# Kernel tuning notes

Hardware: AMD Instinct MI355X
Metric: run time of the kernel (lower is better)

The kernel has to match this reference:

```python
import jax, jax.numpy as jnp
import numpy as np

N_NODES = 50000
N_EDGES = 800000
D = 128
H = 8
HD = D // H
N_NTYPES = 3
N_ETYPES = 5
LN_EPS = 1e-5


def setup_inputs() -> dict:
    key = jax.random.key(0)
    ks = jax.random.split(key, 16)
    inp = {
        "x": jax.random.normal(ks[0], (N_NODES, D), dtype=jnp.float32),
        "edge_index": jax.random.randint(ks[1], (2, N_EDGES), 0, N_NODES),
        "edge_type": jax.random.randint(ks[2], (N_EDGES,), 0, N_ETYPES),
        "node_type": jax.random.randint(ks[3], (N_NODES,), 0, N_NTYPES),
        # per-(node_type, head) QKV projections, per-(edge_type, head) K transform
        "W_Q": jax.random.normal(ks[4], (N_NTYPES, H, HD, HD), dtype=jnp.float32) * 0.02,
        "W_K": jax.random.normal(ks[5], (N_NTYPES, H, HD, HD), dtype=jnp.float32) * 0.02,
        "W_V": jax.random.normal(ks[6], (N_NTYPES, H, HD, HD), dtype=jnp.float32) * 0.02,
        "W_edge": jax.random.normal(ks[7], (N_ETYPES, H, HD, HD), dtype=jnp.float32) * 0.02,
        "mu": jnp.ones((H, N_ETYPES), dtype=jnp.float32),
        "W_out": jax.random.normal(ks[8], (D, D), dtype=jnp.float32) * 0.02,
        "b_out": jnp.zeros((D,), dtype=jnp.float32),
        "ln1_g": jnp.ones((D,), dtype=jnp.float32),
        "ln1_b": jnp.zeros((D,), dtype=jnp.float32),
        "W1": jax.random.normal(ks[9], (D, 4 * D), dtype=jnp.float32) * 0.02,
        "b1": jnp.zeros((4 * D,), dtype=jnp.float32),
        "W2": jax.random.normal(ks[10], (4 * D, D), dtype=jnp.float32) * 0.02,
        "b2": jnp.zeros((D,), dtype=jnp.float32),
        "ln2_g": jnp.ones((D,), dtype=jnp.float32),
        "ln2_b": jnp.zeros((D,), dtype=jnp.float32),
    }
    return inp


def _layer_norm(y, g, b):
    m = y.mean(-1, keepdims=True)
    v = ((y - m) ** 2).mean(-1, keepdims=True)
    return (y - m) * jax.lax.rsqrt(v + LN_EPS) * g + b


def reference(x, edge_index, edge_type, node_type,
              W_Q, W_K, W_V, W_edge, mu,
              W_out, b_out, ln1_g, ln1_b, W1, b1, W2, b2, ln2_g, ln2_b):
    N = x.shape[0]
    xh = x.reshape(N, H, HD)  # heads vectorized (concat of per-head slices)

    # type-specific QKV: small fixed loop over node types, masked select
    Q = jnp.zeros_like(xh)
    K = jnp.zeros_like(xh)
    V = jnp.zeros_like(xh)
    for t in range(N_NTYPES):
        m = (node_type == t)[:, None, None]
        Q = jnp.where(m, jnp.einsum('nhd,hdf->nhf', xh, W_Q[t]), Q)
        K = jnp.where(m, jnp.einsum('nhd,hdf->nhf', xh, W_K[t]), K)
        V = jnp.where(m, jnp.einsum('nhd,hdf->nhf', xh, W_V[t]), V)

    src, dst = edge_index[0], edge_index[1]
    q_dst = Q[dst]   # [E,H,HD]
    k_src = K[src]   # [E,H,HD]

    # edge-type-specific K transform
    kt = jnp.zeros_like(k_src)
    for et in range(N_ETYPES):
        m = (edge_type == et)[:, None, None]
        kt = jnp.where(m, jnp.einsum('ehd,hdf->ehf', k_src, W_edge[et]), kt)

    scores = (q_dst * kt).sum(-1) / jnp.sqrt(jnp.float32(HD))  # [E,H]
    scores = scores * mu[:, edge_type].T                       # mu per edge type, per head

    # sparse softmax over incoming edges of each dst node, per head
    smax = jax.ops.segment_max(scores, dst, num_segments=N)
    ex = jnp.exp(scores - smax[dst])
    den = jax.ops.segment_sum(ex, dst, num_segments=N)
    w = ex / (den[dst] + 1e-10)                                 # [E,H]

    agg = jax.ops.segment_sum(V[src] * w[..., None], dst, num_segments=N)  # [N,H,HD]
    mh = agg.reshape(N, D) @ W_out + b_out  # dropout is identity in eval

    h = _layer_norm(x + mh, ln1_g, ln1_b)
    ffn = jax.nn.gelu(h @ W1 + b1, approximate=False) @ W2 + b2
    return _layer_norm(h + ffn, ln2_g, ln2_b)
```

## Files before the change

### kernel.cpp

```cpp
#include <hip/hip_runtime.h>
#include <hip/hip_bf16.h>

#define N_NODESC 50000
#define N_EDGESC 800000
#define DD 128
#define HH 8
#define HDIM 16
#define N_NT 3
#define N_ET 5
#define NPB 196
#define NEB 400
#define NFB 512

#define KV8_OFF    ((size_t)0)
#define QT8_OFF    ((size_t)12800000)
#define XP_OFF     ((size_t)44800000)
#define AGG_OFF    ((size_t)57600000)
#define WOUTT_OFF  ((size_t)83200000)
#define W1T_OFF    ((size_t)83232768)
#define W2T_OFF    ((size_t)83363840)
#define WALL_OFF   ((size_t)83494912)
#define EDATA_OFF  ((size_t)84183040)
#define ROWS_OFF   ((size_t)87383040)
#define ORIG_OFF   ((size_t)87583104)
#define DEG_OFF    ((size_t)87783104)
#define TOFS_OFF   ((size_t)87983104)
#define BH_OFF     ((size_t)87983168)
#define BB_OFF     ((size_t)87985536)
#define TMP_OFF    ((size_t)87988928)
#define RLOC_OFF   ((size_t)91188928)
#define CSUM_OFF   ((size_t)91389056)

using short8 = __attribute__((ext_vector_type(8))) short;
using f32x4  = __attribute__((ext_vector_type(4))) float;
using f32x2  = __attribute__((ext_vector_type(2))) float;

__device__ __forceinline__ ushort f2b(float f) {
    __hip_bfloat16 h = __float2bfloat16(f);
    return *(ushort*)&h;
}
__device__ __forceinline__ float b2f(ushort u) {
    __hip_bfloat16 h = *(__hip_bfloat16*)&u;
    return __bfloat162float(h);
}
__device__ __forceinline__ f32x2 pk0(unsigned int w) {
    return __builtin_amdgcn_cvt_pk_f32_fp8((int)w, false);
}
__device__ __forceinline__ f32x2 pk1(unsigned int w) {
    return __builtin_amdgcn_cvt_pk_f32_fp8((int)w, true);
}
__device__ __forceinline__ float gelu_f(float v) {
    return 0.5f * v * (1.f + erff(v * 0.70710678118654752f));
}

__global__ __launch_bounds__(256) void prep_a(
    const float* __restrict__ Wout, const float* __restrict__ W1, const float* __restrict__ W2,
    const float* __restrict__ WQ, const float* __restrict__ Wk, const float* __restrict__ Wv,
    const float* __restrict__ We, const float* __restrict__ mu,
    ushort* __restrict__ Woutt, ushort* __restrict__ W1t, ushort* __restrict__ W2t,
    ushort* __restrict__ Wall,
    const int* __restrict__ ntype, int* __restrict__ bh,
    const int* __restrict__ dst, int* __restrict__ deg, unsigned int* __restrict__ tmp)
{
    const int b = blockIdx.x, tid = threadIdx.x;
    if (b < 1920) {
        const int gid = b * 256 + tid;
        if (gid < 16384) {
            const int nn = gid >> 7, k = gid & 127;
            Woutt[gid] = f2b(Wout[k * 128 + nn]);
        } else if (gid < 81920) {
            const int i = gid - 16384;
            const int nn = i >> 7, k = i & 127;
            W1t[i] = f2b(W1[k * 512 + nn]);
        } else if (gid < 147456) {
            const int i = gid - 81920;
            const int nn = i >> 9, k = i & 511;
            W2t[i] = f2b(W2[k * 128 + nn]);
        } else {
            const int idx = gid - 147456;
            const int t = idx / (896 * 128);
            const int rem = idx % (896 * 128);
            const int c = rem / 128, k = rem % 128;
            const int hk = k >> 4, ck = k & 15;
            float v = 0.f;
            if (c < 128) {
                const int hc = c >> 4, j = c & 15;
                if (hk == hc) v = 4.f * Wk[((t * HH + hc) * HDIM + ck) * HDIM + j];
            } else if (c < 256) {
                const int c2 = c - 128, hc = c2 >> 4, j = c2 & 15;
                if (hk == hc) v = 4.f * Wv[((t * HH + hc) * HDIM + ck) * HDIM + j];
            } else {
                const int cq = c - 256, et = cq >> 7, dd = cq & 127;
                const int hq = dd >> 4, j = dd & 15;
                if (hk == hq) {
                    const float* wq = WQ + ((t * HH + hq) * HDIM + ck) * HDIM;
                    const float* we = We + ((et * HH + hq) * HDIM + j) * HDIM;
                    float s = 0.f;
#pragma unroll
                    for (int f = 0; f < 16; f++) s = fmaf(wq[f], we[f], s);
                    v = 64.f * mu[hq * N_ET + et] * s;
                }
            }
            Wall[idx] = f2b(v);
        }
    } else if (b < 1920 + NPB) {
        const int bc = b - 1920;
        const int wave = tid >> 6, lane = tid & 63;
        const int n = bc * 256 + tid;
        const int t = (n < N_NODESC) ? ntype[n] : -1;
        const unsigned long long m0 = __ballot(t == 0);
        const unsigned long long m1 = __ballot(t == 1);
        const unsigned long long m2 = __ballot(t == 2);
        __shared__ int wcnt[4][3];
        if (lane == 0) {
            wcnt[wave][0] = (int)__popcll(m0);
            wcnt[wave][1] = (int)__popcll(m1);
            wcnt[wave][2] = (int)__popcll(m2);
        }
        __syncthreads();
        if (tid < 3)
            bh[tid * NPB + bc] = wcnt[0][tid] + wcnt[1][tid] + wcnt[2][tid] + wcnt[3][tid];
    } else {
        for (int e = (b - 1920 - NPB) * 256 + tid; e < N_EDGESC; e += NEB * 256) {
            const int nd = dst[e];
            const unsigned int p = (unsigned int)atomicAdd(&deg[nd], 1);
            tmp[e] = (p << 16) | (unsigned int)nd;
        }
    }
}

__global__ __launch_bounds__(256) void prep_b(
    const int* __restrict__ bh, const int* __restrict__ deg,
    int* __restrict__ bb, int* __restrict__ tofs,
    int* __restrict__ rloc, int* __restrict__ csum)
{
    __shared__ int part[256];
    const int tid = threadIdx.x;
    if (blockIdx.x == 0) {
        const int base3 = tid * 3;
        int e0 = (base3 + 0 < 588) ? bh[base3 + 0] : 0;
        int e1 = (base3 + 1 < 588) ? bh[base3 + 1] : 0;
        int e2 = (base3 + 2 < 588) ? bh[base3 + 2] : 0;
        const int l0 = e0, l1 = e0 + e1, l2 = l1 + e2;
        part[tid] = l2;
        __syncthreads();
        for (int off = 1; off < 256; off <<= 1) {
            const int u = (tid >= off) ? part[tid - off] : 0;
            __syncthreads();
            part[tid] += u;
            __syncthreads();
        }
        const int tb = part[tid] - l2;
        if (base3 + 0 < 588) bb[base3 + 0] = tb;
        if (base3 + 1 < 588) bb[base3 + 1] = tb + l0;
        if (base3 + 2 < 588) bb[base3 + 2] = tb + l1;
        __syncthreads();
        if (tid == 0) {
            tofs[0] = 0;
            tofs[1] = bb[NPB];
            tofs[2] = bb[2 * NPB];
            tofs[3] = N_NODESC;
        }
    } else {
        const int c = blockIdx.x - 1;
        const int n = c * 256 + tid;
        const int vdeg = (n < N_NODESC) ? deg[n] : 0;
        part[tid] = vdeg;
        __syncthreads();
        for (int off = 1; off < 256; off <<= 1) {
            const int u = (tid >= off) ? part[tid - off] : 0;
            __syncthreads();
            part[tid] += u;
            __syncthreads();
        }
        if (n <= N_NODESC) rloc[n] = part[tid] - vdeg;
        if (tid == 255) csum[c] = part[255];
    }
}

__global__ __launch_bounds__(256) void prep_c(
    const int* __restrict__ ntype, const float* __restrict__ x,
    const int* __restrict__ src, const int* __restrict__ etype,
    const int* __restrict__ bb, const int* __restrict__ rloc, const int* __restrict__ csum,
    const unsigned int* __restrict__ tmp,
    int* __restrict__ origof, ushort* __restrict__ Xp, int* __restrict__ rows,
    int* __restrict__ edata)
{
    const int b = blockIdx.x, tid = threadIdx.x;
    __shared__ int cb[256];
    {
        const int v = (tid < NPB) ? csum[tid] : 0;
        cb[tid] = v;
        __syncthreads();
        for (int off = 1; off < 256; off <<= 1) {
            const int u = (tid >= off) ? cb[tid - off] : 0;
            __syncthreads();
            cb[tid] += u;
            __syncthreads();
        }
        const int incl = cb[tid];
        __syncthreads();
        cb[tid] = incl - v;
        __syncthreads();
    }

    if (b < NPB) {
        const int wave = tid >> 6, lane = tid & 63;
        const int n = b * 256 + tid;
        const int t = (n < N_NODESC) ? ntype[n] : -1;
        const unsigned long long m0 = __ballot(t == 0);
        const unsigned long long m1 = __ballot(t == 1);
        const unsigned long long m2 = __ballot(t == 2);
        __shared__ int wcnt[4][3];
        __shared__ int sp[256];
        if (lane == 0) {
            wcnt[wave][0] = (int)__popcll(m0);
            wcnt[wave][1] = (int)__popcll(m1);
            wcnt[wave][2] = (int)__popcll(m2);
        }
        __syncthreads();
        int p = -1;
        if (n < N_NODESC) {
            int basew = 0;
#pragma unroll
            for (int w = 0; w < 4; w++) if (w < wave) basew += wcnt[w][t];
            const unsigned long long mt = (t == 0) ? m0 : (t == 1) ? m1 : m2;
            const unsigned long long mlt = ((unsigned long long)1 << lane) - 1;
            p = bb[t * NPB + b] + basew + (int)__popcll(mt & mlt);
            origof[p] = n;
        }
        if (n <= N_NODESC) rows[n] = cb[b] + rloc[n];
        sp[tid] = p;
        __syncthreads();
        for (int i = tid; i < 256 * 16; i += 256) {
            const int nn = i >> 4, c = (i & 15) << 3;
            const int pp = sp[nn];
            if (pp < 0) continue;
            const int n2 = b * 256 + nn;
            const float4 v0 = *(const float4*)(x + (size_t)n2 * DD + c);
            const float4 v1 = *(const float4*)(x + (size_t)n2 * DD + c + 4);
            ushort o[8] = {f2b(v0.x), f2b(v0.y), f2b(v0.z), f2b(v0.w),
                           f2b(v1.x), f2b(v1.y), f2b(v1.z), f2b(v1.w)};
            *(uint4*)(Xp + (size_t)pp * DD + c) = *(uint4*)o;
        }
    } else {
        for (int e = (b - NPB) * 256 + tid; e < N_EDGESC; e += NFB * 256) {
            const unsigned int v = tmp[e];
            const int nd = (int)(v & 0xffffu);
            const int p = (int)(v >> 16);
            edata[cb[nd >> 8] + rloc[nd] + p] = src[e] | (etype[e] << 16);
        }
    }
}

#define LDP 36

__global__ __launch_bounds__(256) void proj_gemm(
    const ushort* __restrict__ Xp, const ushort* __restrict__ Wall,
    const int* __restrict__ tofs, const int* __restrict__ origof,
    ushort* __restrict__ KV8, unsigned char* __restrict__ Qt8)
{
    const int t = blockIdx.z;
    const int rs = tofs[t], re = tofs[t + 1];
    const int mBase = rs + blockIdx.x * 128;
    if (mBase >= re) return;
    const int nBase = blockIdx.y * 128;
    const ushort* Bt = Wall + (size_t)t * 896 * 128;

    __shared__ ushort As[128 * LDP];
    __shared__ ushort Bs[128 * LDP];
    const int tid = threadIdx.x;
    const int lane = tid & 63, wave = tid >> 6;
    const int mw = (wave >> 1) * 64, nw = (wave & 1) * 64;
    const int l15 = lane & 15, q8 = (lane >> 4) * 8;

    f32x4 acc[4][4];
#pragma unroll
    for (int i = 0; i < 4; i++)
#pragma unroll
        for (int j = 0; j < 4; j++) acc[i][j] = (f32x4){0.f, 0.f, 0.f, 0.f};

    const int r0 = tid >> 2, c0 = (tid & 3) * 8;
    int rA0 = mBase + r0;      if (rA0 >= N_NODESC) rA0 = N_NODESC - 1;
    int rA1 = mBase + r0 + 64; if (rA1 >= N_NODESC) rA1 = N_NODESC - 1;

    for (int kk = 0; kk < 128; kk += 32) {
        short8 a0 = *(const short8*)(Xp + (size_t)rA0 * DD + kk + c0);
        short8 a1 = *(const short8*)(Xp + (size_t)rA1 * DD + kk + c0);
        short8 b0 = *(const short8*)(Bt + (size_t)(nBase + r0) * 128 + kk + c0);
        short8 b1 = *(const short8*)(Bt + (size_t)(nBase + r0 + 64) * 128 + kk + c0);
        *(short8*)&As[r0 * LDP + c0] = a0;
        *(short8*)&As[(r0 + 64) * LDP + c0] = a1;
        *(short8*)&Bs[r0 * LDP + c0] = b0;
        *(short8*)&Bs[(r0 + 64) * LDP + c0] = b1;
        __syncthreads();
        short8 af[4], bf[4];
#pragma unroll
        for (int i = 0; i < 4; i++)
            af[i] = *(const short8*)&As[(mw + i * 16 + l15) * LDP + q8];
#pragma unroll
        for (int j = 0; j < 4; j++)
            bf[j] = *(const short8*)&Bs[(nw + j * 16 + l15) * LDP + q8];
#pragma unroll
        for (int i = 0; i < 4; i++)
#pragma unroll
            for (int j = 0; j < 4; j++)
                acc[i][j] = __builtin_amdgcn_mfma_f32_16x16x32_bf16(af[i], bf[j], acc[i][j], 0, 0, 0);
        __syncthreads();
    }

    unsigned char* kvb = (unsigned char*)KV8;
    const int rq = (lane >> 4) * 4;
#pragma unroll
    for (int i = 0; i < 4; i++) {
#pragma unroll
        for (int r = 0; r < 4; r++) {
            const int gm = mBase + mw + i * 16 + rq + r;
            if (gm >= re) continue;
            const int og = origof[gm];
#pragma unroll
            for (int j = 0; j < 4; j++) {
                const int gn = nBase + nw + j * 16 + l15;
                const float v = acc[i][j][r];
                const unsigned char b8 =
                    (unsigned char)(__builtin_amdgcn_cvt_pk_fp8_f32(v, v, 0, false) & 0xff);
                if (gn < 256) kvb[(size_t)og * 256 + gn] = b8;
                else          Qt8[(size_t)og * 640 + (gn - 256)] = b8;
            }
        }
    }
}

__global__ __launch_bounds__(128) void edgeagg_kernel(
    const int* __restrict__ rowstart, const int* __restrict__ edata,
    const unsigned char* __restrict__ Qt8, const unsigned char* __restrict__ KV8,
    ushort* __restrict__ agg)
{
    const int w = threadIdx.x >> 6;
    const int lane = threadIdx.x & 63;
    const int n = blockIdx.x * 2 + w;
    const int slot = lane >> 3;
    const int h = lane & 7;

    __shared__ uint4 qs8s[2][40];
    if (lane < 40)
        qs8s[w][lane] = ((const uint4*)(Qt8 + (size_t)n * 640))[lane];
    __syncthreads();
    const uint* qbase = (const uint*)&qs8s[w][0];

    const int s0 = rowstart[n], s1 = rowstart[n + 1];
    const float qsc = 1.44269504f / 1024.f;

    float acc[16];
#pragma unroll
    for (int j = 0; j < 16; j++) acc[j] = 0.f;
    float den = 0.f;

    for (int i = s0 + slot; i < s1; i += 8) {
        const int ed = edata[i];
        const int sn = ed & 0xffff;
        const int et = ed >> 16;
        const unsigned char* kvp = KV8 + ((size_t)sn << 8);
        const uint4 kw = *(const uint4*)(kvp + (h << 4));
        const uint4 vw = *(const uint4*)(kvp + 128 + (h << 4));
        const uint4 qw = *(const uint4*)(qbase + (et << 5) + (h << 2));

        const f32x2 q0 = pk0(qw.x), q1 = pk1(qw.x), q2 = pk0(qw.y), q3 = pk1(qw.y);
        const f32x2 q4 = pk0(qw.z), q5 = pk1(qw.z), q6 = pk0(qw.w), q7 = pk1(qw.w);
        const f32x2 k0 = pk0(kw.x), k1 = pk1(kw.x), k2 = pk0(kw.y), k3 = pk1(kw.y);
        const f32x2 k4 = pk0(kw.z), k5 = pk1(kw.z), k6 = pk0(kw.w), k7 = pk1(kw.w);

        float pa = q0.x * k0.x;
        float pb = q0.y * k0.y;
        float pc = q1.x * k1.x;
        float pd = q1.y * k1.y;
        pa = fmaf(q2.x, k2.x, pa); pb = fmaf(q2.y, k2.y, pb);
        pc = fmaf(q3.x, k3.x, pc); pd = fmaf(q3.y, k3.y, pd);
        pa = fmaf(q4.x, k4.x, pa); pb = fmaf(q4.y, k4.y, pb);
        pc = fmaf(q5.x, k5.x, pc); pd = fmaf(q5.y, k5.y, pd);
        pa = fmaf(q6.x, k6.x, pa); pb = fmaf(q6.y, k6.y, pb);
        pc = fmaf(q7.x, k7.x, pc); pd = fmaf(q7.y, k7.y, pd);

        const float ex = exp2f(((pa + pb) + (pc + pd)) * qsc);
        den += ex;

        const f32x2 v0 = pk0(vw.x), v1 = pk1(vw.x), v2 = pk0(vw.y), v3 = pk1(vw.y);
        const f32x2 v4 = pk0(vw.z), v5 = pk1(vw.z), v6 = pk0(vw.w), v7 = pk1(vw.w);
        acc[0]  = fmaf(ex, v0.x, acc[0]);  acc[1]  = fmaf(ex, v0.y, acc[1]);
        acc[2]  = fmaf(ex, v1.x, acc[2]);  acc[3]  = fmaf(ex, v1.y, acc[3]);
        acc[4]  = fmaf(ex, v2.x, acc[4]);  acc[5]  = fmaf(ex, v2.y, acc[5]);
        acc[6]  = fmaf(ex, v3.x, acc[6]);  acc[7]  = fmaf(ex, v3.y, acc[7]);
        acc[8]  = fmaf(ex, v4.x, acc[8]);  acc[9]  = fmaf(ex, v4.y, acc[9]);
        acc[10] = fmaf(ex, v5.x, acc[10]); acc[11] = fmaf(ex, v5.y, acc[11]);
        acc[12] = fmaf(ex, v6.x, acc[12]); acc[13] = fmaf(ex, v6.y, acc[13]);
        acc[14] = fmaf(ex, v7.x, acc[14]); acc[15] = fmaf(ex, v7.y, acc[15]);
    }

    {
        const int b0 = slot & 1, b1 = slot & 2, b2 = slot & 4;
#pragma unroll
        for (int j = 0; j < 8; j++) {
            const float v = b0 ? acc[j] : acc[j + 8];
            const float r = __shfl_xor(v, 8);
            acc[j] = (b0 ? acc[j + 8] : acc[j]) + r;
        }
#pragma unroll
        for (int j = 0; j < 4; j++) {
            const float v = b1 ? acc[j] : acc[j + 4];
            const float r = __shfl_xor(v, 16);
            acc[j] = (b1 ? acc[j + 4] : acc[j]) + r;
        }
#pragma unroll
        for (int j = 0; j < 2; j++) {
            const float v = b2 ? acc[j] : acc[j + 2];
            const float r = __shfl_xor(v, 32);
            acc[j] = (b2 ? acc[j + 2] : acc[j]) + r;
        }
        den += __shfl_xor(den, 8);
        den += __shfl_xor(den, 16);
        den += __shfl_xor(den, 32);
    }
    const float rr = 0.25f / (den + 1e-10f);
    const int fb = (h << 4) + ((slot & 1) << 3) + ((slot & 2) << 1) + ((slot & 4) >> 1);
    ushort o2[2] = { f2b(acc[0] * rr), f2b(acc[1] * rr) };
    *(uint*)&agg[((size_t)n << 7) + fb] = *(uint*)o2;
}

#define LDH 132

__global__ __launch_bounds__(256) void fused_tail(
    const ushort* __restrict__ agg, const ushort* __restrict__ Woutt,
    const ushort* __restrict__ W1t, const ushort* __restrict__ W2t,
    const float* __restrict__ x,
    const float* __restrict__ bout, const float* __restrict__ g1, const float* __restrict__ b1ln,
    const float* __restrict__ b1, const float* __restrict__ b2,
    const float* __restrict__ g2, const float* __restrict__ b2ln,
    float* __restrict__ out)
{
    __shared__ ushort Hs[64 * LDH];
    __shared__ ushort As[64 * LDP];
    __shared__ ushort Bs[128 * LDP];
    __shared__ float red[2][2][64];

    const int tid = threadIdx.x;
    const int lane = tid & 63, wave = tid >> 6;
    const int wm = wave >> 1, wn = wave & 1;
    const int l15 = lane & 15, q8 = (lane >> 4) * 8, rq = (lane >> 4) * 4;
    const int mBase = blockIdx.x * 64;

    const int rA = tid >> 2, c0 = (tid & 3) * 8;
    int rowA = mBase + rA; if (rowA >= N_NODESC) rowA = N_NODESC - 1;

    f32x4 acc1[2][4], acc2[2][4];
#pragma unroll
    for (int i = 0; i < 2; i++)
#pragma unroll
        for (int j = 0; j < 4; j++) {
            acc1[i][j] = (f32x4){0.f, 0.f, 0.f, 0.f};
            acc2[i][j] = (f32x4){0.f, 0.f, 0.f, 0.f};
        }

    for (int kk = 0; kk < 128; kk += 32) {
        short8 a0 = *(const short8*)(agg + (size_t)rowA * DD + kk + c0);
        short8 b0 = *(const short8*)(Woutt + (size_t)rA * 128 + kk + c0);
        short8 b1r = *(const short8*)(Woutt + (size_t)(rA + 64) * 128 + kk + c0);
        *(short8*)&As[rA * LDP + c0] = a0;
        *(short8*)&Bs[rA * LDP + c0] = b0;
        *(short8*)&Bs[(rA + 64) * LDP + c0] = b1r;
        __syncthreads();
        short8 af[2], bf[4];
#pragma unroll
        for (int i = 0; i < 2; i++)
            af[i] = *(const short8*)&As[(wm * 32 + i * 16 + l15) * LDP + q8];
#pragma unroll
        for (int j = 0; j < 4; j++)
            bf[j] = *(const short8*)&Bs[(wn * 64 + j * 16 + l15) * LDP + q8];
#pragma unroll
        for (int i = 0; i < 2; i++)
#pragma unroll
            for (int j = 0; j < 4; j++)
                acc1[i][j] = __builtin_amdgcn_mfma_f32_16x16x32_bf16(af[i], bf[j], acc1[i][j], 0, 0, 0);
        __syncthreads();
    }

    {
        float boutv[4], gv[4], bv[4];
#pragma unroll
        for (int j = 0; j < 4; j++) {
            const int gn = wn * 64 + j * 16 + l15;
            boutv[j] = bout[gn]; gv[j] = g1[gn]; bv[j] = b1ln[gn];
        }
#pragma unroll
        for (int i = 0; i < 2; i++) {
#pragma unroll
            for (int r = 0; r < 4; r++) {
                const int row = wm * 32 + i * 16 + rq + r;
                const int gm = mBase + row;
                float s = 0.f, ss = 0.f;
#pragma unroll
                for (int j = 0; j < 4; j++) {
                    const int gn = wn * 64 + j * 16 + l15;
                    float v = acc1[i][j][r] + boutv[j];
                    v += (gm < N_NODESC) ? x[(size_t)gm * DD + gn] : 0.f;
                    acc1[i][j][r] = v;
                    s += v; ss += v * v;
                }
                s  += __shfl_xor(s, 1);  s  += __shfl_xor(s, 2);  s  += __shfl_xor(s, 4);  s  += __shfl_xor(s, 8);
                ss += __shfl_xor(ss, 1); ss += __shfl_xor(ss, 2); ss += __shfl_xor(ss, 4); ss += __shfl_xor(ss, 8);
                if (l15 == 0) { red[0][wn][row] = s; red[1][wn][row] = ss; }
            }
        }
        __syncthreads();
#pragma unroll
        for (int i = 0; i < 2; i++) {
#pragma unroll
            for (int r = 0; r < 4; r++) {
                const int row = wm * 32 + i * 16 + rq + r;
                const float s  = red[0][0][row] + red[0][1][row];
                const float ss = red[1][0][row] + red[1][1][row];
                const float mean = s * (1.f / 128.f);
                const float var  = ss * (1.f / 128.f) - mean * mean;
                const float rstd = rsqrtf(var + 1e-5f);
#pragma unroll
                for (int j = 0; j < 4; j++) {
                    const int gn = wn * 64 + j * 16 + l15;
                    const float o = (acc1[i][j][r] - mean) * rstd * gv[j] + bv[j];
                    Hs[row * LDH + gn] = f2b(o);
                }
            }
        }
        __syncthreads();
    }

    for (int nb = 0; nb < 4; nb++) {
#pragma unroll
        for (int i = 0; i < 2; i++)
#pragma unroll
            for (int j = 0; j < 4; j++) acc1[i][j] = (f32x4){0.f, 0.f, 0.f, 0.f};

        for (int kk = 0; kk < 128; kk += 32) {
            short8 b0 = *(const short8*)(W1t + (size_t)(nb * 128 + rA) * 128 + kk + c0);
            short8 b1r = *(const short8*)(W1t + (size_t)(nb * 128 + rA + 64) * 128 + kk + c0);
            *(short8*)&Bs[rA * LDP + c0] = b0;
            *(short8*)&Bs[(rA + 64) * LDP + c0] = b1r;
            __syncthreads();
            short8 af[2], bf[4];
#pragma unroll
            for (int i = 0; i < 2; i++)
                af[i] = *(const short8*)&Hs[(wm * 32 + i * 16 + l15) * LDH + kk + q8];
#pragma unroll
            for (int j = 0; j < 4; j++)
                bf[j] = *(const short8*)&Bs[(wn * 64 + j * 16 + l15) * LDP + q8];
#pragma unroll
            for (int i = 0; i < 2; i++)
#pragma unroll
                for (int j = 0; j < 4; j++)
                    acc1[i][j] = __builtin_amdgcn_mfma_f32_16x16x32_bf16(af[i], bf[j], acc1[i][j], 0, 0, 0);
            __syncthreads();
        }

        float b1v[4];
#pragma unroll
        for (int j = 0; j < 4; j++)
            b1v[j] = b1[nb * 128 + wn * 64 + j * 16 + l15];

        for (int kk2 = 0; kk2 < 4; kk2++) {
            short8 b0 = *(const short8*)(W2t + (size_t)rA * 512 + nb * 128 + kk2 * 32 + c0);
            short8 b1r = *(const short8*)(W2t + (size_t)(rA + 64) * 512 + nb * 128 + kk2 * 32 + c0);
            *(short8*)&Bs[rA * LDP + c0] = b0;
            *(short8*)&Bs[(rA + 64) * LDP + c0] = b1r;
            if (wn == (kk2 >> 1)) {
                const int j0 = 2 * (kk2 & 1);
#pragma unroll
                for (int i = 0; i < 2; i++)
#pragma unroll
                    for (int jj = 0; jj < 2; jj++)
#pragma unroll
                        for (int r = 0; r < 4; r++) {
                            const int row = wm * 32 + i * 16 + rq + r;
                            const float v = gelu_f(acc1[i][j0 + jj][r] + b1v[j0 + jj]);
                            As[row * LDP + jj * 16 + l15] = f2b(v);
                        }
            }
            __syncthreads();
            short8 af[2], bf[4];
#pragma unroll
            for (int i = 0; i < 2; i++)
                af[i] = *(const short8*)&As[(wm * 32 + i * 16 + l15) * LDP + q8];
#pragma unroll
            for (int j = 0; j < 4; j++)
                bf[j] = *(const short8*)&Bs[(wn * 64 + j * 16 + l15) * LDP + q8];
#pragma unroll
            for (int i = 0; i < 2; i++)
#pragma unroll
                for (int j = 0; j < 4; j++)
                    acc2[i][j] = __builtin_amdgcn_mfma_f32_16x16x32_bf16(af[i], bf[j], acc2[i][j], 0, 0, 0);
            __syncthreads();
        }
    }

    {
        float b2v[4], gv[4], bv[4];
#pragma unroll
        for (int j = 0; j < 4; j++) {
            const int gn = wn * 64 + j * 16 + l15;
            b2v[j] = b2[gn]; gv[j] = g2[gn]; bv[j] = b2ln[gn];
        }
#pragma unroll
        for (int i = 0; i < 2; i++) {
#pragma unroll
            for (int r = 0; r < 4; r++) {
                const int row = wm * 32 + i * 16 + rq + r;
                float s = 0.f, ss = 0.f;
#pragma unroll
                for (int j = 0; j < 4; j++) {
                    const int gn = wn * 64 + j * 16 + l15;
                    float v = acc2[i][j][r] + b2v[j] + b2f(Hs[row * LDH + gn]);
                    acc2[i][j][r] = v;
                    s += v; ss += v * v;
                }
                s  += __shfl_xor(s, 1);  s  += __shfl_xor(s, 2);  s  += __shfl_xor(s, 4);  s  += __shfl_xor(s, 8);
                ss += __shfl_xor(ss, 1); ss += __shfl_xor(ss, 2); ss += __shfl_xor(ss, 4); ss += __shfl_xor(ss, 8);
                if (l15 == 0) { red[0][wn][row] = s; red[1][wn][row] = ss; }
            }
        }
        __syncthreads();
#pragma unroll
        for (int i = 0; i < 2; i++) {
#pragma unroll
            for (int r = 0; r < 4; r++) {
                const int row = wm * 32 + i * 16 + rq + r;
                const int gm = mBase + row;
                if (gm >= N_NODESC) continue;
                const float s  = red[0][0][row] + red[0][1][row];
                const float ss = red[1][0][row] + red[1][1][row];
                const float mean = s * (1.f / 128.f);
                const float var  = ss * (1.f / 128.f) - mean * mean;
                const float rstd = rsqrtf(var + 1e-5f);
#pragma unroll
                for (int j = 0; j < 4; j++) {
                    const int gn = wn * 64 + j * 16 + l15;
                    out[(size_t)gm * DD + gn] = (acc2[i][j][r] - mean) * rstd * gv[j] + bv[j];
                }
            }
        }
    }
}

extern "C" void kernel_launch(void* const* d_in, const int* in_sizes, int n_in,
                              void* d_out, int out_size, void* d_ws, size_t ws_size,
                              hipStream_t stream)
{
    const float* x     = (const float*)d_in[0];
    const int*   ei    = (const int*)d_in[1];
    const int*   etyp  = (const int*)d_in[2];
    const int*   ntype = (const int*)d_in[3];
    const float* Wq    = (const float*)d_in[4];
    const float* Wk    = (const float*)d_in[5];
    const float* Wv    = (const float*)d_in[6];
    const float* We    = (const float*)d_in[7];
    const float* mu    = (const float*)d_in[8];
    const float* Wout  = (const float*)d_in[9];
    const float* bout  = (const float*)d_in[10];
    const float* g1    = (const float*)d_in[11];
    const float* b1ln  = (const float*)d_in[12];
    const float* W1    = (const float*)d_in[13];
    const float* b1    = (const float*)d_in[14];
    const float* W2    = (const float*)d_in[15];
    const float* b2    = (const float*)d_in[16];
    const float* g2    = (const float*)d_in[17];
    const float* b2ln  = (const float*)d_in[18];
    float* out = (float*)d_out;

    char* ws = (char*)d_ws;
    ushort*        KV8   = (ushort*)(ws + KV8_OFF);
    unsigned char* Qt8   = (unsigned char*)(ws + QT8_OFF);
    ushort*        Xp    = (ushort*)(ws + XP_OFF);
    ushort*        agg   = (ushort*)(ws + AGG_OFF);
    ushort*        Woutt = (ushort*)(ws + WOUTT_OFF);
    ushort*        W1t   = (ushort*)(ws + W1T_OFF);
    ushort*        W2t   = (ushort*)(ws + W2T_OFF);
    ushort*        Wall  = (ushort*)(ws + WALL_OFF);
    int*           edata = (int*)(ws + EDATA_OFF);
    int*           rows  = (int*)(ws + ROWS_OFF);
    int*           origof= (int*)(ws + ORIG_OFF);
    int*           deg   = (int*)(ws + DEG_OFF);
    int*           tofs  = (int*)(ws + TOFS_OFF);
    int*           bh    = (int*)(ws + BH_OFF);
    int*           bb    = (int*)(ws + BB_OFF);
    unsigned int*  tmp   = (unsigned int*)(ws + TMP_OFF);
    int*           rloc  = (int*)(ws + RLOC_OFF);
    int*           csum  = (int*)(ws + CSUM_OFF);

    const int* srcA = ei;
    const int* dstA = ei + N_EDGESC;

    (void)hipMemsetAsync(ws + DEG_OFF, 0, 200000, stream);

    prep_a<<<1920 + NPB + NEB, 256, 0, stream>>>(
        Wout, W1, W2, Wq, Wk, Wv, We, mu, Woutt, W1t, W2t, Wall,
        ntype, bh, dstA, deg, tmp);
    prep_b<<<1 + NPB, 256, 0, stream>>>(bh, deg, bb, tofs, rloc, csum);
    prep_c<<<NPB + NFB, 256, 0, stream>>>(ntype, x, srcA, etyp, bb, rloc, csum, tmp,
                                          origof, Xp, rows, edata);

    proj_gemm<<<dim3(394, 7, 3), 256, 0, stream>>>(Xp, Wall, tofs, origof, KV8, Qt8);
    edgeagg_kernel<<<N_NODESC / 2, 128, 0, stream>>>(rows, edata, Qt8,
                                                     (const unsigned char*)KV8, agg);

    fused_tail<<<782, 256, 0, stream>>>(agg, Woutt, W1t, W2t, x,
                                        bout, g1, b1ln, b1, b2, g2, b2ln, out);
}
```

Baseline: 342.4 us.

## Prefetch next weight tiles into registers and stage full GELU tile in LDS

Restructures the fused tail kernel so each k-step issues the global loads for the next weight/agg tile into registers before computing on the current LDS tile. The loads chain across the Wout, W1 and W2 phases. Barriers become a custom ebar that waits only on LDS counters, leaving global loads in flight across it. The GELU output of each W1 block is written to a new full 64x128 Ts buffer in one pass instead of half-tile slices per W2 step. This costs more LDS and can lower occupancy.

```diff
diff --git a/kernel.cpp b/kernel.cpp
--- a/kernel.cpp
+++ b/kernel.cpp
@@ -51,6 +51,13 @@
 }
 __device__ __forceinline__ float gelu_f(float v) {
     return 0.5f * v * (1.f + erff(v * 0.70710678118654752f));
+}
+__device__ __forceinline__ void ebar() {
+    __builtin_amdgcn_sched_barrier(0);
+    asm volatile("s_waitcnt lgkmcnt(0)" ::: "memory");
+    __builtin_amdgcn_sched_barrier(0);
+    __builtin_amdgcn_s_barrier();
+    __builtin_amdgcn_sched_barrier(0);
 }
 
 __global__ __launch_bounds__(256) void prep_a(
@@ -437,9 +444,10 @@
     const float* __restrict__ g2, const float* __restrict__ b2ln,
     float* __restrict__ out)
 {
-    __shared__ ushort Hs[64 * LDH];
     __shared__ ushort As[64 * LDP];
     __shared__ ushort Bs[128 * LDP];
+    __shared__ ushort Hs[64 * LDH];
+    __shared__ ushort Ts[64 * LDH];
     __shared__ float red[2][2][64];
 
     const int tid = threadIdx.x;
@@ -448,8 +456,8 @@
     const int l15 = lane & 15, q8 = (lane >> 4) * 8, rq = (lane >> 4) * 4;
     const int mBase = blockIdx.x * 64;
 
-    const int rA = tid >> 2, c0 = (tid & 3) * 8;
-    int rowA = mBase + rA; if (rowA >= N_NODESC) rowA = N_NODESC - 1;
+    const int r0 = tid >> 2, c0 = (tid & 3) * 8;
+    int rowA = mBase + r0; if (rowA >= N_NODESC) rowA = N_NODESC - 1;
 
     f32x4 acc1[2][4], acc2[2][4];
 #pragma unroll
@@ -460,14 +468,25 @@
             acc2[i][j] = (f32x4){0.f, 0.f, 0.f, 0.f};
         }
 
-    for (int kk = 0; kk < 128; kk += 32) {
-        short8 a0 = *(const short8*)(agg + (size_t)rowA * DD + kk + c0);
-        short8 b0 = *(const short8*)(Woutt + (size_t)rA * 128 + kk + c0);
-        short8 b1r = *(const short8*)(Woutt + (size_t)(rA + 64) * 128 + kk + c0);
-        *(short8*)&As[rA * LDP + c0] = a0;
-        *(short8*)&Bs[rA * LDP + c0] = b0;
-        *(short8*)&Bs[(rA + 64) * LDP + c0] = b1r;
-        __syncthreads();
+    short8 pA, pB0, pB1;
+    pA  = *(const short8*)(agg + (size_t)rowA * DD + c0);
+    pB0 = *(const short8*)(Woutt + (size_t)r0 * 128 + c0);
+    pB1 = *(const short8*)(Woutt + (size_t)(r0 + 64) * 128 + c0);
+
+    for (int kk = 0; kk < 4; kk++) {
+        ebar();
+        *(short8*)&As[r0 * LDP + c0] = pA;
+        *(short8*)&Bs[r0 * LDP + c0] = pB0;
+        *(short8*)&Bs[(r0 + 64) * LDP + c0] = pB1;
+        if (kk < 3) {
+            pA  = *(const short8*)(agg + (size_t)rowA * DD + (kk + 1) * 32 + c0);
+            pB0 = *(const short8*)(Woutt + (size_t)r0 * 128 + (kk + 1) * 32 + c0);
+            pB1 = *(const short8*)(Woutt + (size_t)(r0 + 64) * 128 + (kk + 1) * 32 + c0);
+        } else {
+            pB0 = *(const short8*)(W1t + (size_t)r0 * 128 + c0);
+            pB1 = *(const short8*)(W1t + (size_t)(r0 + 64) * 128 + c0);
+        }
+        ebar();
         short8 af[2], bf[4];
 #pragma unroll
         for (int i = 0; i < 2; i++)
@@ -480,7 +499,6 @@
 #pragma unroll
             for (int j = 0; j < 4; j++)
                 acc1[i][j] = __builtin_amdgcn_mfma_f32_16x16x32_bf16(af[i], bf[j], acc1[i][j], 0, 0, 0);
-        __syncthreads();
     }
 
     {
@@ -496,12 +514,12 @@
             for (int r = 0; r < 4; r++) {
                 const int row = wm * 32 + i * 16 + rq + r;
                 const int gm = mBase + row;
+                const int gr = (gm < N_NODESC) ? gm : N_NODESC - 1;
                 float s = 0.f, ss = 0.f;
 #pragma unroll
                 for (int j = 0; j < 4; j++) {
                     const int gn = wn * 64 + j * 16 + l15;
-                    float v = acc1[i][j][r] + boutv[j];
-                    v += (gm < N_NODESC) ? x[(size_t)gm * DD + gn] : 0.f;
+                    float v = acc1[i][j][r] + boutv[j] + x[(size_t)gr * DD + gn];
                     acc1[i][j][r] = v;
                     s += v; ss += v * v;
                 }
@@ -510,7 +528,7 @@
                 if (l15 == 0) { red[0][wn][row] = s; red[1][wn][row] = ss; }
             }
         }
-        __syncthreads();
+        ebar();
 #pragma unroll
         for (int i = 0; i < 2; i++) {
 #pragma unroll
@@ -524,30 +542,35 @@
 #pragma unroll
                 for (int j = 0; j < 4; j++) {
                     const int gn = wn * 64 + j * 16 + l15;
-                    const float o = (acc1[i][j][r] - mean) * rstd * gv[j] + bv[j];
-                    Hs[row * LDH + gn] = f2b(o);
+                    Hs[row * LDH + gn] = f2b((acc1[i][j][r] - mean) * rstd * gv[j] + bv[j]);
                 }
             }
         }
-        __syncthreads();
     }
 
     for (int nb = 0; nb < 4; nb++) {
+        f32x4 a1[2][4];
 #pragma unroll
         for (int i = 0; i < 2; i++)
 #pragma unroll
-            for (int j = 0; j < 4; j++) acc1[i][j] = (f32x4){0.f, 0.f, 0.f, 0.f};
-
-        for (int kk = 0; kk < 128; kk += 32) {
-            short8 b0 = *(const short8*)(W1t + (size_t)(nb * 128 + rA) * 128 + kk + c0);
-            short8 b1r = *(const short8*)(W1t + (size_t)(nb * 128 + rA + 64) * 128 + kk + c0);
-            *(short8*)&Bs[rA * LDP + c0] = b0;
-            *(short8*)&Bs[(rA + 64) * LDP + c0] = b1r;
-            __syncthreads();
+            for (int j = 0; j < 4; j++) a1[i][j] = (f32x4){0.f, 0.f, 0.f, 0.f};
+
+        for (int kk = 0; kk < 4; kk++) {
+            ebar();
+            *(short8*)&Bs[r0 * LDP + c0] = pB0;
+            *(short8*)&Bs[(r0 + 64) * LDP + c0] = pB1;
+            if (kk < 3) {
+                pB0 = *(const short8*)(W1t + (size_t)(nb * 128 + r0) * 128 + (kk + 1) * 32 + c0);
+                pB1 = *(const short8*)(W1t + (size_t)(nb * 128 + r0 + 64) * 128 + (kk + 1) * 32 + c0);
+            } else {
+                pB0 = *(const short8*)(W2t + (size_t)r0 * 512 + nb * 128 + c0);
+                pB1 = *(const short8*)(W2t + (size_t)(r0 + 64) * 512 + nb * 128 + c0);
+            }
+            ebar();
             short8 af[2], bf[4];
 #pragma unroll
             for (int i = 0; i < 2; i++)
-                af[i] = *(const short8*)&Hs[(wm * 32 + i * 16 + l15) * LDH + kk + q8];
+                af[i] = *(const short8*)&Hs[(wm * 32 + i * 16 + l15) * LDH + kk * 32 + q8];
 #pragma unroll
             for (int j = 0; j < 4; j++)
                 bf[j] = *(const short8*)&Bs[(wn * 64 + j * 16 + l15) * LDP + q8];
@@ -555,38 +578,42 @@
             for (int i = 0; i < 2; i++)
 #pragma unroll
                 for (int j = 0; j < 4; j++)
-                    acc1[i][j] = __builtin_amdgcn_mfma_f32_16x16x32_bf16(af[i], bf[j], acc1[i][j], 0, 0, 0);
-            __syncthreads();
-        }
-
-        float b1v[4];
-#pragma unroll
-        for (int j = 0; j < 4; j++)
-            b1v[j] = b1[nb * 128 + wn * 64 + j * 16 + l15];
-
-        for (int kk2 = 0; kk2 < 4; kk2++) {
-            short8 b0 = *(const short8*)(W2t + (size_t)rA * 512 + nb * 128 + kk2 * 32 + c0);
-            short8 b1r = *(const short8*)(W2t + (size_t)(rA + 64) * 512 + nb * 128 + kk2 * 32 + c0);
-            *(short8*)&Bs[rA * LDP + c0] = b0;
-            *(short8*)&Bs[(rA + 64) * LDP + c0] = b1r;
-            if (wn == (kk2 >> 1)) {
-                const int j0 = 2 * (kk2 & 1);
-#pragma unroll
-                for (int i = 0; i < 2; i++)
-#pragma unroll
-                    for (int jj = 0; jj < 2; jj++)
-#pragma unroll
-                        for (int r = 0; r < 4; r++) {
-                            const int row = wm * 32 + i * 16 + rq + r;
-                            const float v = gelu_f(acc1[i][j0 + jj][r] + b1v[j0 + jj]);
-                            As[row * LDP + jj * 16 + l15] = f2b(v);
-                        }
+                    a1[i][j] = __builtin_amdgcn_mfma_f32_16x16x32_bf16(af[i], bf[j], a1[i][j], 0, 0, 0);
+        }
+
+        {
+            float b1v[4];
+#pragma unroll
+            for (int j = 0; j < 4; j++)
+                b1v[j] = b1[nb * 128 + wn * 64 + j * 16 + l15];
+#pragma unroll
+            for (int i = 0; i < 2; i++)
+#pragma unroll
+                for (int j = 0; j < 4; j++)
+#pragma unroll
+                    for (int r = 0; r < 4; r++) {
+                        const int row = wm * 32 + i * 16 + rq + r;
+                        const int col = wn * 64 + j * 16 + l15;
+                        Ts[row * LDH + col] = f2b(gelu_f(a1[i][j][r] + b1v[j]));
+                    }
+        }
+
+        for (int kk = 0; kk < 4; kk++) {
+            ebar();
+            *(short8*)&Bs[r0 * LDP + c0] = pB0;
+            *(short8*)&Bs[(r0 + 64) * LDP + c0] = pB1;
+            if (kk < 3) {
+                pB0 = *(const short8*)(W2t + (size_t)r0 * 512 + nb * 128 + (kk + 1) * 32 + c0);
+                pB1 = *(const short8*)(W2t + (size_t)(r0 + 64) * 512 + nb * 128 + (kk + 1) * 32 + c0);
+            } else if (nb < 3) {
+                pB0 = *(const short8*)(W1t + (size_t)((nb + 1) * 128 + r0) * 128 + c0);
+                pB1 = *(const short8*)(W1t + (size_t)((nb + 1) * 128 + r0 + 64) * 128 + c0);
             }
-            __syncthreads();
+            ebar();
             short8 af[2], bf[4];
 #pragma unroll
             for (int i = 0; i < 2; i++)
-                af[i] = *(const short8*)&As[(wm * 32 + i * 16 + l15) * LDP + q8];
+                af[i] = *(const short8*)&Ts[(wm * 32 + i * 16 + l15) * LDH + kk * 32 + q8];
 #pragma unroll
             for (int j = 0; j < 4; j++)
                 bf[j] = *(const short8*)&Bs[(wn * 64 + j * 16 + l15) * LDP + q8];
@@ -595,7 +622,6 @@
 #pragma unroll
                 for (int j = 0; j < 4; j++)
                     acc2[i][j] = __builtin_amdgcn_mfma_f32_16x16x32_bf16(af[i], bf[j], acc2[i][j], 0, 0, 0);
-            __syncthreads();
         }
     }
 
@@ -606,6 +632,7 @@
             const int gn = wn * 64 + j * 16 + l15;
             b2v[j] = b2[gn]; gv[j] = g2[gn]; bv[j] = b2ln[gn];
         }
+        ebar();
 #pragma unroll
         for (int i = 0; i < 2; i++) {
 #pragma unroll
@@ -624,7 +651,7 @@
                 if (l15 == 0) { red[0][wn][row] = s; red[1][wn][row] = ss; }
             }
         }
-        __syncthreads();
+        ebar();
 #pragma unroll
         for (int i = 0; i < 2; i++) {
 #pragma unroll
```

Result: faster. 324.8 us (-5.1%).
